# Optimization experiments

Measured on AMD Instinct MI355X. Metric: run time of the kernel, lower is better.

The kernel has to match this reference:

```python
import jax, jax.numpy as jnp
import numpy as np
from jax import lax


def setup_inputs() -> dict:
    key = jax.random.key(0)
    k1, k2, k3 = jax.random.split(key, 3)
    B, C, H, W = 32, 256, 64, 64
    E, O, K = 4, 256, 3
    x = jax.random.normal(k1, (B, C, H, W), dtype=jnp.float32)
    router_w = jax.random.normal(k2, (E, C, 1, 1), dtype=jnp.float32) * 0.02
    router_b = jnp.zeros((E,), dtype=jnp.float32)
    expert_w = jax.random.normal(k3, (E, O, C, K, K), dtype=jnp.float32) * 0.05
    return {"x": x, "router_w": router_w, "router_b": router_b, "expert_w": expert_w}


def reference(x, router_w, router_b, expert_w):
    # x: [B, C, H, W]; router_w: [E, C, 1, 1]; expert_w: [E, O, C, K, K]
    B, C, H, W = x.shape
    E, O, _, K, _ = expert_w.shape

    # Router: global average pool -> 1x1 conv -> softmax over experts
    pooled = jnp.mean(x, axis=(2, 3))                       # [B, C]
    logits = jnp.einsum('bc,ec->be', pooled, router_w.reshape(E, C)) + router_b
    attn = jax.nn.softmax(logits, axis=1)                   # [B, E]

    # CondConv equivalence: sum_e attn[b,e]*conv_e(x_b) == conv(x_b, sum_e attn[b,e]*W_e)
    w_b = jnp.einsum('be,eocij->bocij', attn, expert_w)     # [B, O, C, K, K]

    # Per-sample kernels via a single grouped conv (groups = B)
    xg = x.reshape(1, B * C, H, W)                          # [1, B*C, H, W]
    wg = w_b.reshape(B * O, C, K, K)                        # [B*O, C, K, K]
    y = lax.conv_general_dilated(
        xg, wg,
        window_strides=(1, 1),
        padding=[(K // 2, K // 2), (K // 2, K // 2)],
        feature_group_count=B,
        dimension_numbers=('NCHW', 'OIHW', 'NCHW'),
    )                                                        # [1, B*O, H, W]
    return y.reshape(B, O, H, W)
```

## Files before the change

### kernel.cpp

```cpp
#include <hip/hip_runtime.h>
#include <hip/hip_bf16.h>
#include <stdint.h>

#define NB 32
#define NC 256
#define NH 64
#define NW 64
#define NE 4
#define NO 256

typedef __bf16 bf16x8 __attribute__((ext_vector_type(8)));
typedef float  f32x4  __attribute__((ext_vector_type(4)));

__device__ __forceinline__ unsigned short f2bf(float f) {
  union { float f; uint32_t u; } v; v.f = f;
  uint32_t u = v.u;
  uint32_t r = (u + 0x7FFFu + ((u >> 16) & 1u)) >> 16;
  return (unsigned short)r;
}


__global__ __launch_bounds__(256) void xt_k(const float* __restrict__ x,
                                            unsigned short* __restrict__ xT,
                                            float* __restrict__ rowsum) {
  const int bh = blockIdx.x;
  const int tid = threadIdx.x;
  const int ci = tid >> 4;
  const int wq = (tid & 15) * 4;
  __shared__ unsigned short t_lds[256 * 66];

#pragma unroll 4
  for (int p = 0; p < 16; ++p) {
    const int c = p * 16 + ci;
    const float4 v = *(const float4*)&x[(((size_t)(blockIdx.x >> 6) * 256 + c) * 64 +
                                         (bh & 63)) * 64 + wq];
    uint32_t p0 = (uint32_t)f2bf(v.x) | ((uint32_t)f2bf(v.y) << 16);
    uint32_t p1 = (uint32_t)f2bf(v.z) | ((uint32_t)f2bf(v.w) << 16);
    *(uint32_t*)&t_lds[c * 66 + wq]     = p0;
    *(uint32_t*)&t_lds[c * 66 + wq + 2] = p1;
    float s = (v.x + v.y) + (v.z + v.w);
    s += __shfl_down(s, 8, 16);
    s += __shfl_down(s, 4, 16);
    s += __shfl_down(s, 2, 16);
    s += __shfl_down(s, 1, 16);
    if ((tid & 15) == 0) rowsum[((size_t)bh << 8) + c] = s;
  }
  __syncthreads();
#pragma unroll
  for (int i = 0; i < 8; ++i) {
    const int m  = tid + (i << 8);
    const int w  = m >> 5;
    const int cg = m & 31;
    uint32_t q0 = (uint32_t)t_lds[(cg * 8 + 0) * 66 + w] |
                  ((uint32_t)t_lds[(cg * 8 + 1) * 66 + w] << 16);
    uint32_t q1 = (uint32_t)t_lds[(cg * 8 + 2) * 66 + w] |
                  ((uint32_t)t_lds[(cg * 8 + 3) * 66 + w] << 16);
    uint32_t q2 = (uint32_t)t_lds[(cg * 8 + 4) * 66 + w] |
                  ((uint32_t)t_lds[(cg * 8 + 5) * 66 + w] << 16);
    uint32_t q3 = (uint32_t)t_lds[(cg * 8 + 6) * 66 + w] |
                  ((uint32_t)t_lds[(cg * 8 + 7) * 66 + w] << 16);
    uint4 q = {q0, q1, q2, q3};
    *(uint4*)&xT[(((size_t)bh << 6) + w) * 256 + cg * 8] = q;
  }
}

__global__ __launch_bounds__(256) void router2_k(const float* __restrict__ rowsum,
                                                 const float* __restrict__ rw,
                                                 const float* __restrict__ rb,
                                                 float* __restrict__ attn,
                                                 uint32_t* __restrict__ zpage) {
  const int b = blockIdx.x, tid = threadIdx.x;
  if (b == 0) { uint4 z = {0, 0, 0, 0}; ((uint4*)zpage)[tid] = z; }
  float s = 0.f;
#pragma unroll 8
  for (int h = 0; h < 64; ++h) s += rowsum[((size_t)(b * 64 + h) << 8) + tid];
  __shared__ float pl[256];
  __shared__ float lg[4];
  pl[tid] = s * (1.f / 4096.f);
  __syncthreads();
  const int e = tid >> 6, ln = tid & 63;
  float d = pl[ln]       * rw[e * 256 + ln] +
            pl[ln + 64]  * rw[e * 256 + ln + 64] +
            pl[ln + 128] * rw[e * 256 + ln + 128] +
            pl[ln + 192] * rw[e * 256 + ln + 192];
#pragma unroll
  for (int off = 32; off > 0; off >>= 1) d += __shfl_down(d, off, 64);
  if (ln == 0) lg[e] = d + rb[e];
  __syncthreads();
  if (tid == 0) {
    float l0 = lg[0], l1 = lg[1], l2 = lg[2], l3 = lg[3];
    float m  = fmaxf(fmaxf(l0, l1), fmaxf(l2, l3));
    float e0 = expf(l0 - m), e1 = expf(l1 - m), e2 = expf(l2 - m), e3 = expf(l3 - m);
    float inv = 1.f / (e0 + e1 + e2 + e3);
    attn[b * 4 + 0] = e0 * inv;
    attn[b * 4 + 1] = e1 * inv;
    attn[b * 4 + 2] = e2 * inv;
    attn[b * 4 + 3] = e3 * inv;
  }
}

__global__ __launch_bounds__(256) void wmix_k2(const float* __restrict__ ew,
                                               const float* __restrict__ attn,
                                               unsigned short* __restrict__ wmix) {
  __shared__ float at[128];
  if (threadIdx.x < 128) at[threadIdx.x] = attn[threadIdx.x];
  __syncthreads();
  const int i   = blockIdx.x * 256 + threadIdx.x;
  const int c32 = i & 31;
  const int o   = (i >> 5) & 255;
  const int cb  = (i >> 13) & 7;
  const int t   = i >> 16;
  const int c   = cb * 32 + c32;
  const size_t estride = (size_t)NO * NC * 9;
  const size_t wi = ((size_t)o * NC + c) * 9 + t;
  const float e0 = ew[wi], e1 = ew[wi + estride], e2 = ew[wi + 2 * estride],
              e3 = ew[wi + 3 * estride];
  const size_t outbase = ((size_t)t * 8 + cb) * 8192 + o * 32 + c32;
#pragma unroll 4
  for (int b = 0; b < 32; ++b) {
    float s = at[b * 4] * e0 + at[b * 4 + 1] * e1 + at[b * 4 + 2] * e2 +
              at[b * 4 + 3] * e3;
    wmix[outbase + (size_t)b * 589824] = f2bf(s);
  }
}

__global__ __launch_bounds__(256, 2) void conv_k2(
    const unsigned short* __restrict__ xT, const unsigned short* __restrict__ wmix,
    const unsigned short* __restrict__ zpage, float* __restrict__ y) {
  const int bid   = blockIdx.x;
  const int r     = bid >> 3;
  const int ptile = r & 31;
  const int ob    = ((r >> 5) & 1) * 128;
  const int b     = (bid & 7) + ((r >> 6) << 3);
  const int tid   = threadIdx.x;
  const int lane  = tid & 63;
  const int wid   = tid >> 6;
  const int wm    = (wid >> 1) * 64;
  const int wrow  = wid & 1;
  const int h0    = ptile * 2;
  const int lm    = lane & 15;
  const int lq    = lane >> 4;

  __shared__ unsigned short xlds[2][8704];

  const unsigned short* sptr[5];
  uint32_t cbadd[5];
#pragma unroll
  for (int i = 0; i < 5; ++i) {
    const int chunk = wid + 4 * i;
    const int d   = chunk * 64 + lane;
    const int row = d / 264;
    const int rem = d - row * 264;
    const int col = rem >> 2;
    const int s   = rem & 3;
    const int g   = s ^ ((col >> 1) & 3);
    const int gh  = h0 - 1 + row;
    const int w   = col - 1;
    const bool ok = (d < 1056) && (gh >= 0) && (gh < NH) && (w >= 0) && (w < NW);
    sptr[i]  = ok ? xT + (((size_t)((b * 64 + gh) * 64 + w)) << 8) + g * 8
                  : zpage + lane * 8;
    cbadd[i] = ok ? 32u : 0u;
  }

  auto stage = [&](int cbv, int buf) {
#pragma unroll
    for (int i = 0; i < 5; ++i) {
      if (wid + 4 * i < 17) {
        const unsigned short* src = sptr[i] + cbadd[i] * (uint32_t)cbv;
        char* dst = (char*)&xlds[buf][0] + (wid + 4 * i) * 1024;
        __builtin_amdgcn_global_load_lds(
            (const __attribute__((address_space(1))) void*)src,
            (__attribute__((address_space(3))) void*)dst, 16, 0, 0);
      }
    }
  };

  uint32_t xpo[3][4];
#pragma unroll
  for (int kw = 0; kw < 3; ++kw)
#pragma unroll
    for (int nf = 0; nf < 4; ++nf) {
      const int col = nf * 16 + lm + kw;
      xpo[kw][nf] = (uint32_t)(wrow * 4224) + ((uint32_t)col << 6) |
                    ((uint32_t)(lq ^ ((col >> 1) & 3)) << 4);
    }

  f32x4 acc[4][4];
#pragma unroll
  for (int i = 0; i < 4; ++i)
#pragma unroll
    for (int j = 0; j < 4; ++j) acc[i][j] = {0.f, 0.f, 0.f, 0.f};

  const unsigned short* wptr =
      wmix + (size_t)b * 589824 + (ob + wm + lm) * 32 + lq * 8;

#define LOADW(d0, d1, d2, d3, delta)                                          \
  {                                                                           \
    d0 = *(const bf16x8*)(wptr);                                              \
    d1 = *(const bf16x8*)(wptr + 512);                                        \
    d2 = *(const bf16x8*)(wptr + 1024);                                       \
    d3 = *(const bf16x8*)(wptr + 1536);                                       \
    wptr += (delta);                                                          \
  }

#define LOADX(d0, d1, d2, d3, XQ, khimm)                                      \
  {                                                                           \
    d0 = *(const bf16x8*)(XQ[0] + (khimm));                                   \
    d1 = *(const bf16x8*)(XQ[1] + (khimm));                                   \
    d2 = *(const bf16x8*)(XQ[2] + (khimm));                                   \
    d3 = *(const bf16x8*)(XQ[3] + (khimm));                                   \
  }

#define MFMA16(W0, W1, W2, W3, X0, X1, X2, X3)                                      \
  __builtin_amdgcn_s_setprio(1);                                                   \
  acc[0][0] = __builtin_amdgcn_mfma_f32_16x16x32_bf16(W0, X0, acc[0][0], 0, 0, 0); \
  acc[0][1] = __builtin_amdgcn_mfma_f32_16x16x32_bf16(W0, X1, acc[0][1], 0, 0, 0); \
  acc[0][2] = __builtin_amdgcn_mfma_f32_16x16x32_bf16(W0, X2, acc[0][2], 0, 0, 0); \
  acc[0][3] = __builtin_amdgcn_mfma_f32_16x16x32_bf16(W0, X3, acc[0][3], 0, 0, 0); \
  acc[1][0] = __builtin_amdgcn_mfma_f32_16x16x32_bf16(W1, X0, acc[1][0], 0, 0, 0); \
  acc[1][1] = __builtin_amdgcn_mfma_f32_16x16x32_bf16(W1, X1, acc[1][1], 0, 0, 0); \
  acc[1][2] = __builtin_amdgcn_mfma_f32_16x16x32_bf16(W1, X2, acc[1][2], 0, 0, 0); \
  acc[1][3] = __builtin_amdgcn_mfma_f32_16x16x32_bf16(W1, X3, acc[1][3], 0, 0, 0); \
  acc[2][0] = __builtin_amdgcn_mfma_f32_16x16x32_bf16(W2, X0, acc[2][0], 0, 0, 0); \
  acc[2][1] = __builtin_amdgcn_mfma_f32_16x16x32_bf16(W2, X1, acc[2][1], 0, 0, 0); \
  acc[2][2] = __builtin_amdgcn_mfma_f32_16x16x32_bf16(W2, X2, acc[2][2], 0, 0, 0); \
  acc[2][3] = __builtin_amdgcn_mfma_f32_16x16x32_bf16(W2, X3, acc[2][3], 0, 0, 0); \
  acc[3][0] = __builtin_amdgcn_mfma_f32_16x16x32_bf16(W3, X0, acc[3][0], 0, 0, 0); \
  acc[3][1] = __builtin_amdgcn_mfma_f32_16x16x32_bf16(W3, X1, acc[3][1], 0, 0, 0); \
  acc[3][2] = __builtin_amdgcn_mfma_f32_16x16x32_bf16(W3, X2, acc[3][2], 0, 0, 0); \
  acc[3][3] = __builtin_amdgcn_mfma_f32_16x16x32_bf16(W3, X3, acc[3][3], 0, 0, 0); \
  __builtin_amdgcn_s_setprio(0);

#define SB __builtin_amdgcn_sched_barrier(0);

  bf16x8 wa0, wa1, wa2, wa3, wb0, wb1, wb2, wb3, wc0, wc1, wc2, wc3;
  bf16x8 xc0, xc1, xc2, xc3, xn0, xn1, xn2, xn3;
  stage(0, 0);
  LOADW(wa0, wa1, wa2, wa3, 65536);
  LOADW(wb0, wb1, wb2, wb3, 65536);
  __syncthreads();

  for (int cb = 0; cb < 8; ++cb) {
    if (cb < 7) stage(cb + 1, (cb & 1) ^ 1);
    const char* xb = (const char*)&xlds[cb & 1][0];
    const char* xq0[4];
    const char* xq1[4];
    const char* xq2[4];
#pragma unroll
    for (int nf = 0; nf < 4; ++nf) {
      xq0[nf] = xb + xpo[0][nf];
      xq1[nf] = xb + xpo[1][nf];
      xq2[nf] = xb + xpo[2][nf];
    }
    LOADX(xc0, xc1, xc2, xc3, xq0, 0);
    LOADW(wc0, wc1, wc2, wc3, 65536);
    LOADX(xn0, xn1, xn2, xn3, xq1, 0);
    SB MFMA16(wa0, wa1, wa2, wa3, xc0, xc1, xc2, xc3)
    LOADW(wa0, wa1, wa2, wa3, 65536);
    LOADX(xc0, xc1, xc2, xc3, xq2, 0);
    SB MFMA16(wb0, wb1, wb2, wb3, xn0, xn1, xn2, xn3)
    LOADW(wb0, wb1, wb2, wb3, 65536);
    LOADX(xn0, xn1, xn2, xn3, xq0, 4224);
    SB MFMA16(wc0, wc1, wc2, wc3, xc0, xc1, xc2, xc3)
    LOADW(wc0, wc1, wc2, wc3, 65536);
    LOADX(xc0, xc1, xc2, xc3, xq1, 4224);
    SB MFMA16(wa0, wa1, wa2, wa3, xn0, xn1, xn2, xn3)
    LOADW(wa0, wa1, wa2, wa3, 65536);
    LOADX(xn0, xn1, xn2, xn3, xq2, 4224);
    SB MFMA16(wb0, wb1, wb2, wb3, xc0, xc1, xc2, xc3)
    LOADW(wb0, wb1, wb2, wb3, 65536);
    LOADX(xc0, xc1, xc2, xc3, xq0, 8448);
    SB MFMA16(wc0, wc1, wc2, wc3, xn0, xn1, xn2, xn3)
    LOADW(wc0, wc1, wc2, wc3, -516096);
    LOADX(xn0, xn1, xn2, xn3, xq1, 8448);
    SB MFMA16(wa0, wa1, wa2, wa3, xc0, xc1, xc2, xc3)
    LOADW(wa0, wa1, wa2, wa3, 65536);
    LOADX(xc0, xc1, xc2, xc3, xq2, 8448);
    SB MFMA16(wb0, wb1, wb2, wb3, xn0, xn1, xn2, xn3)
    LOADW(wb0, wb1, wb2, wb3, 65536);
    SB MFMA16(wc0, wc1, wc2, wc3, xc0, xc1, xc2, xc3)
    asm volatile("s_waitcnt vmcnt(8)" ::: "memory");
    __builtin_amdgcn_s_barrier();
  }

  const int h = h0 + wrow;
#pragma unroll
  for (int mf = 0; mf < 4; ++mf) {
#pragma unroll
    for (int nf = 0; nf < 4; ++nf) {
      f32x4 v = acc[mf][nf];
      const int wcol = nf * 16 + lm;
#pragma unroll
      for (int i = 0; i < 4; ++i) {
        const int o = ob + wm + mf * 16 + lq * 4 + i;
        y[(((size_t)b * NO + o) * NH + h) * NW + wcol] = v[i];
      }
    }
  }
#undef LOADW
#undef LOADX
#undef MFMA16
#undef SB
}


__global__ __launch_bounds__(256) void pool_k(const float* __restrict__ x,
                                              float* __restrict__ pooled) {
  const int bc  = blockIdx.x;
  const int tid = threadIdx.x;
  const float4* base = (const float4*)(x + (size_t)bc * (NH * NW));
  float s = 0.f;
#pragma unroll
  for (int i = 0; i < 4; ++i) {
    float4 v = base[tid + 256 * i];
    s += v.x + v.y + v.z + v.w;
  }
#pragma unroll
  for (int off = 32; off > 0; off >>= 1) s += __shfl_down(s, off, 64);
  __shared__ float ws[4];
  if ((tid & 63) == 0) ws[tid >> 6] = s;
  __syncthreads();
  if (tid == 0) pooled[bc] = (ws[0] + ws[1] + ws[2] + ws[3]) * (1.f / (NH * NW));
}

__global__ __launch_bounds__(64) void router_k(const float* __restrict__ pooled,
                                               const float* __restrict__ rw,
                                               const float* __restrict__ rb,
                                               float* __restrict__ attn) {
  const int b = blockIdx.x, t = threadIdx.x;
  float p0 = 0.f, p1 = 0.f, p2 = 0.f, p3 = 0.f;
  for (int c = t; c < NC; c += 64) {
    float pv = pooled[b * NC + c];
    p0 += pv * rw[0 * NC + c];
    p1 += pv * rw[1 * NC + c];
    p2 += pv * rw[2 * NC + c];
    p3 += pv * rw[3 * NC + c];
  }
#pragma unroll
  for (int off = 32; off > 0; off >>= 1) {
    p0 += __shfl_down(p0, off, 64);
    p1 += __shfl_down(p1, off, 64);
    p2 += __shfl_down(p2, off, 64);
    p3 += __shfl_down(p3, off, 64);
  }
  if (t == 0) {
    float l0 = p0 + rb[0], l1 = p1 + rb[1], l2 = p2 + rb[2], l3 = p3 + rb[3];
    float m  = fmaxf(fmaxf(l0, l1), fmaxf(l2, l3));
    float e0 = expf(l0 - m), e1 = expf(l1 - m), e2 = expf(l2 - m), e3 = expf(l3 - m);
    float inv = 1.f / (e0 + e1 + e2 + e3);
    attn[b * 4 + 0] = e0 * inv;
    attn[b * 4 + 1] = e1 * inv;
    attn[b * 4 + 2] = e2 * inv;
    attn[b * 4 + 3] = e3 * inv;
  }
}

__global__ __launch_bounds__(256) void conv_k(const float* __restrict__ x,
                                              const unsigned short* __restrict__ wmix,
                                              float* __restrict__ y) {
  const int ptile = blockIdx.x;
  const int ob    = blockIdx.y * 128;
  const int b     = blockIdx.z;
  const int tid   = threadIdx.x;
  const int lane  = tid & 63;
  const int wid   = tid >> 6;
  const int wm    = (wid >> 1) * 64;
  const int wrow  = wid & 1;
  const int h0    = ptile * 2;
  const int lm = lane & 15;
  const int lq = lane >> 4;
  const int g8 = lq * 8;

  __shared__ unsigned short xlds[4 * 66 * 32];
  __shared__ unsigned short wlds[2][128 * 32];

  f32x4 acc[4][4];
#pragma unroll
  for (int i = 0; i < 4; ++i)
#pragma unroll
    for (int j = 0; j < 4; ++j) acc[i][j] = {0.f, 0.f, 0.f, 0.f};

  const int sr  = tid >> 6;
  const int scp = tid & 15;
  const int scg = (tid >> 4) & 3;
  const int gh  = h0 - 1 + sr;
  const bool hok = (gh >= 0) && (gh < NH);

  for (int cb = 0; cb < 8; ++cb) {
    {
      const float* xr0 =
          x + (((size_t)(b * NC + cb * 32 + 2 * scp) * NH + (hok ? gh : 0)) * NW);
      const float* xr1 = xr0 + (size_t)NH * NW;
      for (int k = 0; k < 17; ++k) {
        int col = scg + 4 * k;
        if (col < 66) {
          int w   = col - 1;
          bool ok = hok && (w >= 0) && (w < NW);
          float f0 = ok ? xr0[w] : 0.f;
          float f1 = ok ? xr1[w] : 0.f;
          uint32_t pk = (uint32_t)f2bf(f0) | ((uint32_t)f2bf(f1) << 16);
          *(uint32_t*)&xlds[(sr * 66 + col) * 32 + 2 * scp] = pk;
        }
      }
    }
    const size_t wchunk = (size_t)(b * 9) * 65536 + (size_t)cb * 8192 + (size_t)ob * 32;
    auto stageW = [&](int t, int buf) {
      const unsigned short* src = wmix + wchunk + (size_t)t * 65536 + tid * 8;
      char* dst = (char*)&wlds[buf][0] + (tid >> 6) * 1024;
      __builtin_amdgcn_global_load_lds((const __attribute__((address_space(1))) void*)src,
                                       (__attribute__((address_space(3))) void*)dst,
                                       16, 0, 0);
      __builtin_amdgcn_global_load_lds(
          (const __attribute__((address_space(1))) void*)(src + 2048),
          (__attribute__((address_space(3))) void*)(dst + 4096), 16, 0, 0);
    };
    stageW(0, 0);
    __syncthreads();

#pragma unroll
    for (int t = 0; t < 9; ++t) {
      if (t < 8) stageW(t + 1, (t + 1) & 1);
      const int kh = t / 3, kw = t % 3;
      const unsigned short* wb = &wlds[t & 1][0];
      bf16x8 af[4], bfr[4];
#pragma unroll
      for (int mf = 0; mf < 4; ++mf)
        af[mf] = *(const bf16x8*)&wb[(wm + mf * 16 + lm) * 32 + g8];
#pragma unroll
      for (int nf = 0; nf < 4; ++nf)
        bfr[nf] = *(const bf16x8*)&xlds[((wrow + kh) * 66 + (nf * 16 + lm + kw)) * 32 + g8];
#pragma unroll
      for (int mf = 0; mf < 4; ++mf)
#pragma unroll
        for (int nf = 0; nf < 4; ++nf)
          acc[mf][nf] =
              __builtin_amdgcn_mfma_f32_16x16x32_bf16(af[mf], bfr[nf], acc[mf][nf], 0, 0, 0);
      __syncthreads();
    }
  }

  const int h = h0 + wrow;
#pragma unroll
  for (int mf = 0; mf < 4; ++mf) {
#pragma unroll
    for (int nf = 0; nf < 4; ++nf) {
      f32x4 v = acc[mf][nf];
      int wcol = nf * 16 + lm;
#pragma unroll
      for (int i = 0; i < 4; ++i) {
        int o = ob + wm + mf * 16 + lq * 4 + i;
        y[(((size_t)b * NO + o) * NH + h) * NW + wcol] = v[i];
      }
    }
  }
}


extern "C" void kernel_launch(void* const* d_in, const int* in_sizes, int n_in,
                              void* d_out, int out_size, void* d_ws, size_t ws_size,
                              hipStream_t stream) {
  const float* x  = (const float*)d_in[0];
  const float* rw = (const float*)d_in[1];
  const float* rb = (const float*)d_in[2];
  const float* ew = (const float*)d_in[3];
  float* yout = (float*)d_out;

  float* pooled = (float*)d_ws;
  float* attn   = (float*)((char*)d_ws + 32768);
  unsigned short* wmix = (unsigned short*)((char*)d_ws + 65536);
  const size_t OFF_ROWSUM = 65536 + 37748736;
  const size_t OFF_XT     = OFF_ROWSUM + 2097152;
  const size_t OFF_ZERO   = OFF_XT + 67108864;
  const size_t NEED       = OFF_ZERO + 4096;

  if (ws_size >= NEED) {
    float* rowsum = (float*)((char*)d_ws + OFF_ROWSUM);
    unsigned short* xT = (unsigned short*)((char*)d_ws + OFF_XT);
    uint32_t* zpage = (uint32_t*)((char*)d_ws + OFF_ZERO);
    xt_k<<<2048, 256, 0, stream>>>(x, xT, rowsum);
    router2_k<<<32, 256, 0, stream>>>(rowsum, rw, rb, attn, zpage);
    wmix_k2<<<2304, 256, 0, stream>>>(ew, attn, wmix);
    conv_k2<<<2048, 256, 0, stream>>>(xT, wmix, (const unsigned short*)zpage, yout);
  } else {
    pool_k<<<NB * NC, 256, 0, stream>>>(x, pooled);
    router_k<<<NB, 64, 0, stream>>>(pooled, rw, rb, attn);
    wmix_k2<<<2304, 256, 0, stream>>>(ew, attn, wmix);
    conv_k<<<dim3(32, 2, 32), 256, 0, stream>>>(x, wmix, yout);
  }
}
```

Baseline: 223.7 us.

## Split conv block across eight waves with smaller per-wave output tiles

The conv kernel now runs with 512 threads (8 waves) per block instead of 4, and each wave computes a 64x32 output tile instead of 64x64. This halves the accumulator and x-fragment register footprint, so more waves can be resident to hide memory latency, and the LDS staging is spread across more waves. In exchange the weight loads are duplicated across twice as many waves, raising global and L2 traffic per MFMA, and the lower MFMA-to-load ratio may expose more memory latency.

After: 338.1 us. 1.51x slower.

```diff
diff --git a/kernel.cpp b/kernel.cpp
--- a/kernel.cpp
+++ b/kernel.cpp
@@ -124,7 +124,7 @@
   }
 }
 
-__global__ __launch_bounds__(256, 2) void conv_k2(
+__global__ __launch_bounds__(512, 4) void conv_k3(
     const unsigned short* __restrict__ xT, const unsigned short* __restrict__ wmix,
     const unsigned short* __restrict__ zpage, float* __restrict__ y) {
   const int bid   = blockIdx.x;
@@ -135,19 +135,21 @@
   const int tid   = threadIdx.x;
   const int lane  = tid & 63;
   const int wid   = tid >> 6;
-  const int wm    = (wid >> 1) * 64;
-  const int wrow  = wid & 1;
+  const int wm    = (wid >> 2) * 64;
+  const int wn    = (wid & 3) * 32;
+  const int wrow  = wn >> 6;
+  const int col0  = wn & 63;
   const int h0    = ptile * 2;
   const int lm    = lane & 15;
   const int lq    = lane >> 4;
 
   __shared__ unsigned short xlds[2][8704];
 
-  const unsigned short* sptr[5];
-  uint32_t cbadd[5];
-#pragma unroll
-  for (int i = 0; i < 5; ++i) {
-    const int chunk = wid + 4 * i;
+  const unsigned short* sptr[3];
+  uint32_t cbadd[3];
+#pragma unroll
+  for (int i = 0; i < 3; ++i) {
+    const int chunk = wid + 8 * i;
     const int d   = chunk * 64 + lane;
     const int row = d / 264;
     const int rem = d - row * 264;
@@ -164,10 +166,10 @@
 
   auto stage = [&](int cbv, int buf) {
 #pragma unroll
-    for (int i = 0; i < 5; ++i) {
-      if (wid + 4 * i < 17) {
+    for (int i = 0; i < 3; ++i) {
+      if (wid + 8 * i < 17) {
         const unsigned short* src = sptr[i] + cbadd[i] * (uint32_t)cbv;
-        char* dst = (char*)&xlds[buf][0] + (wid + 4 * i) * 1024;
+        char* dst = (char*)&xlds[buf][0] + (wid + 8 * i) * 1024;
         __builtin_amdgcn_global_load_lds(
             (const __attribute__((address_space(1))) void*)src,
             (__attribute__((address_space(3))) void*)dst, 16, 0, 0);
@@ -175,21 +177,22 @@
     }
   };
 
-  uint32_t xpo[3][4];
+  uint32_t xpo[3][2];
 #pragma unroll
   for (int kw = 0; kw < 3; ++kw)
 #pragma unroll
-    for (int nf = 0; nf < 4; ++nf) {
-      const int col = nf * 16 + lm + kw;
-      xpo[kw][nf] = (uint32_t)(wrow * 4224) + ((uint32_t)col << 6) |
-                    ((uint32_t)(lq ^ ((col >> 1) & 3)) << 4);
-    }
-
-  f32x4 acc[4][4];
+    for (int nf = 0; nf < 2; ++nf) {
+      const int col = col0 + nf * 16 + lm + kw;
+      xpo[kw][nf] = (uint32_t)(wrow * 4224) +
+                    (((uint32_t)col << 6) |
+                     ((uint32_t)(lq ^ ((col >> 1) & 3)) << 4));
+    }
+
+  f32x4 acc[4][2];
 #pragma unroll
   for (int i = 0; i < 4; ++i)
 #pragma unroll
-    for (int j = 0; j < 4; ++j) acc[i][j] = {0.f, 0.f, 0.f, 0.f};
+    for (int j = 0; j < 2; ++j) acc[i][j] = {0.f, 0.f, 0.f, 0.f};
 
   const unsigned short* wptr =
       wmix + (size_t)b * 589824 + (ob + wm + lm) * 32 + lq * 8;
@@ -203,38 +206,28 @@
     wptr += (delta);                                                          \
   }
 
-#define LOADX(d0, d1, d2, d3, XQ, khimm)                                      \
+#define LOADX2(d0, d1, kwv, khimm)                                            \
   {                                                                           \
-    d0 = *(const bf16x8*)(XQ[0] + (khimm));                                   \
-    d1 = *(const bf16x8*)(XQ[1] + (khimm));                                   \
-    d2 = *(const bf16x8*)(XQ[2] + (khimm));                                   \
-    d3 = *(const bf16x8*)(XQ[3] + (khimm));                                   \
-  }
-
-#define MFMA16(W0, W1, W2, W3, X0, X1, X2, X3)                                      \
+    d0 = *(const bf16x8*)(xb + xpo[(kwv)][0] + (khimm));                      \
+    d1 = *(const bf16x8*)(xb + xpo[(kwv)][1] + (khimm));                      \
+  }
+
+#define MFMA8(W0, W1, W2, W3, X0, X1)                                               \
   __builtin_amdgcn_s_setprio(1);                                                   \
   acc[0][0] = __builtin_amdgcn_mfma_f32_16x16x32_bf16(W0, X0, acc[0][0], 0, 0, 0); \
   acc[0][1] = __builtin_amdgcn_mfma_f32_16x16x32_bf16(W0, X1, acc[0][1], 0, 0, 0); \
-  acc[0][2] = __builtin_amdgcn_mfma_f32_16x16x32_bf16(W0, X2, acc[0][2], 0, 0, 0); \
-  acc[0][3] = __builtin_amdgcn_mfma_f32_16x16x32_bf16(W0, X3, acc[0][3], 0, 0, 0); \
   acc[1][0] = __builtin_amdgcn_mfma_f32_16x16x32_bf16(W1, X0, acc[1][0], 0, 0, 0); \
   acc[1][1] = __builtin_amdgcn_mfma_f32_16x16x32_bf16(W1, X1, acc[1][1], 0, 0, 0); \
-  acc[1][2] = __builtin_amdgcn_mfma_f32_16x16x32_bf16(W1, X2, acc[1][2], 0, 0, 0); \
-  acc[1][3] = __builtin_amdgcn_mfma_f32_16x16x32_bf16(W1, X3, acc[1][3], 0, 0, 0); \
   acc[2][0] = __builtin_amdgcn_mfma_f32_16x16x32_bf16(W2, X0, acc[2][0], 0, 0, 0); \
   acc[2][1] = __builtin_amdgcn_mfma_f32_16x16x32_bf16(W2, X1, acc[2][1], 0, 0, 0); \
-  acc[2][2] = __builtin_amdgcn_mfma_f32_16x16x32_bf16(W2, X2, acc[2][2], 0, 0, 0); \
-  acc[2][3] = __builtin_amdgcn_mfma_f32_16x16x32_bf16(W2, X3, acc[2][3], 0, 0, 0); \
   acc[3][0] = __builtin_amdgcn_mfma_f32_16x16x32_bf16(W3, X0, acc[3][0], 0, 0, 0); \
   acc[3][1] = __builtin_amdgcn_mfma_f32_16x16x32_bf16(W3, X1, acc[3][1], 0, 0, 0); \
-  acc[3][2] = __builtin_amdgcn_mfma_f32_16x16x32_bf16(W3, X2, acc[3][2], 0, 0, 0); \
-  acc[3][3] = __builtin_amdgcn_mfma_f32_16x16x32_bf16(W3, X3, acc[3][3], 0, 0, 0); \
   __builtin_amdgcn_s_setprio(0);
 
 #define SB __builtin_amdgcn_sched_barrier(0);
 
   bf16x8 wa0, wa1, wa2, wa3, wb0, wb1, wb2, wb3, wc0, wc1, wc2, wc3;
-  bf16x8 xc0, xc1, xc2, xc3, xn0, xn1, xn2, xn3;
+  bf16x8 xc0, xc1, xn0, xn1;
   stage(0, 0);
   LOADW(wa0, wa1, wa2, wa3, 65536);
   LOADW(wb0, wb1, wb2, wb3, 65536);
@@ -243,42 +236,33 @@
   for (int cb = 0; cb < 8; ++cb) {
     if (cb < 7) stage(cb + 1, (cb & 1) ^ 1);
     const char* xb = (const char*)&xlds[cb & 1][0];
-    const char* xq0[4];
-    const char* xq1[4];
-    const char* xq2[4];
-#pragma unroll
-    for (int nf = 0; nf < 4; ++nf) {
-      xq0[nf] = xb + xpo[0][nf];
-      xq1[nf] = xb + xpo[1][nf];
-      xq2[nf] = xb + xpo[2][nf];
-    }
-    LOADX(xc0, xc1, xc2, xc3, xq0, 0);
+    LOADX2(xc0, xc1, 0, 0);
     LOADW(wc0, wc1, wc2, wc3, 65536);
-    LOADX(xn0, xn1, xn2, xn3, xq1, 0);
-    SB MFMA16(wa0, wa1, wa2, wa3, xc0, xc1, xc2, xc3)
+    LOADX2(xn0, xn1, 1, 0);
+    SB MFMA8(wa0, wa1, wa2, wa3, xc0, xc1)
     LOADW(wa0, wa1, wa2, wa3, 65536);
-    LOADX(xc0, xc1, xc2, xc3, xq2, 0);
-    SB MFMA16(wb0, wb1, wb2, wb3, xn0, xn1, xn2, xn3)
+    LOADX2(xc0, xc1, 2, 0);
+    SB MFMA8(wb0, wb1, wb2, wb3, xn0, xn1)
     LOADW(wb0, wb1, wb2, wb3, 65536);
-    LOADX(xn0, xn1, xn2, xn3, xq0, 4224);
-    SB MFMA16(wc0, wc1, wc2, wc3, xc0, xc1, xc2, xc3)
+    LOADX2(xn0, xn1, 0, 4224);
+    SB MFMA8(wc0, wc1, wc2, wc3, xc0, xc1)
     LOADW(wc0, wc1, wc2, wc3, 65536);
-    LOADX(xc0, xc1, xc2, xc3, xq1, 4224);
-    SB MFMA16(wa0, wa1, wa2, wa3, xn0, xn1, xn2, xn3)
+    LOADX2(xc0, xc1, 1, 4224);
+    SB MFMA8(wa0, wa1, wa2, wa3, xn0, xn1)
     LOADW(wa0, wa1, wa2, wa3, 65536);
-    LOADX(xn0, xn1, xn2, xn3, xq2, 4224);
-    SB MFMA16(wb0, wb1, wb2, wb3, xc0, xc1, xc2, xc3)
+    LOADX2(xn0, xn1, 2, 4224);
+    SB MFMA8(wb0, wb1, wb2, wb3, xc0, xc1)
     LOADW(wb0, wb1, wb2, wb3, 65536);
-    LOADX(xc0, xc1, xc2, xc3, xq0, 8448);
-    SB MFMA16(wc0, wc1, wc2, wc3, xn0, xn1, xn2, xn3)
+    LOADX2(xc0, xc1, 0, 8448);
+    SB MFMA8(wc0, wc1, wc2, wc3, xn0, xn1)
     LOADW(wc0, wc1, wc2, wc3, -516096);
-    LOADX(xn0, xn1, xn2, xn3, xq1, 8448);
-    SB MFMA16(wa0, wa1, wa2, wa3, xc0, xc1, xc2, xc3)
+    LOADX2(xn0, xn1, 1, 8448);
+    SB MFMA8(wa0, wa1, wa2, wa3, xc0, xc1)
     LOADW(wa0, wa1, wa2, wa3, 65536);
-    LOADX(xc0, xc1, xc2, xc3, xq2, 8448);
-    SB MFMA16(wb0, wb1, wb2, wb3, xn0, xn1, xn2, xn3)
+    LOADX2(xc0, xc1, 2, 8448);
+    SB MFMA8(wb0, wb1, wb2, wb3, xn0, xn1)
     LOADW(wb0, wb1, wb2, wb3, 65536);
-    SB MFMA16(wc0, wc1, wc2, wc3, xc0, xc1, xc2, xc3)
+    SB MFMA8(wc0, wc1, wc2, wc3, xc0, xc1)
     asm volatile("s_waitcnt vmcnt(8)" ::: "memory");
     __builtin_amdgcn_s_barrier();
   }
@@ -287,9 +271,9 @@
 #pragma unroll
   for (int mf = 0; mf < 4; ++mf) {
 #pragma unroll
-    for (int nf = 0; nf < 4; ++nf) {
+    for (int nf = 0; nf < 2; ++nf) {
       f32x4 v = acc[mf][nf];
-      const int wcol = nf * 16 + lm;
+      const int wcol = col0 + nf * 16 + lm;
 #pragma unroll
       for (int i = 0; i < 4; ++i) {
         const int o = ob + wm + mf * 16 + lq * 4 + i;
@@ -298,8 +282,8 @@
     }
   }
 #undef LOADW
-#undef LOADX
-#undef MFMA16
+#undef LOADX2
+#undef MFMA8
 #undef SB
 }
 
@@ -480,7 +464,7 @@
     xt_k<<<2048, 256, 0, stream>>>(x, xT, rowsum);
     router2_k<<<32, 256, 0, stream>>>(rowsum, rw, rb, attn, zpage);
     wmix_k2<<<2304, 256, 0, stream>>>(ew, attn, wmix);
-    conv_k2<<<2048, 256, 0, stream>>>(xT, wmix, (const unsigned short*)zpage, yout);
+    conv_k3<<<2048, 512, 0, stream>>>(xT, wmix, (const unsigned short*)zpage, yout);
   } else {
     pool_k<<<NB * NC, 256, 0, stream>>>(x, pooled);
     router_k<<<NB, 64, 0, stream>>>(pooled, rw, rb, attn);
```
